# Kernel tuning notes

Hardware: AMD Instinct MI355X
Metric: run time of the kernel (lower is better)

Reference implementation:

```python
import jax, jax.numpy as jnp
import numpy as np
from jax import lax

NUM_TAGS = 19
IN_DIM = 202
HID = 100
B, T = 256, 512


def setup_inputs() -> dict:
    key = jax.random.key(0)
    ks = jax.random.split(key, 16)
    u = lambda k, shape, s: jax.random.uniform(k, shape, jnp.float32, -s, s)
    sh = 1.0 / np.sqrt(HID)
    sl = 1.0 / np.sqrt(2 * HID)
    x = jax.random.normal(ks[0], (B, T, IN_DIM), jnp.float32)
    lengths = jax.random.randint(ks[1], (B,), 1, T + 1)
    raw_tags = jax.random.randint(ks[2], (B, T), 0, NUM_TAGS)
    y = jnp.where(jnp.arange(T)[None, :] < lengths[:, None], raw_tags, -1)
    return dict(
        x=x, y=y,
        w_ih_f=u(ks[3], (HID, IN_DIM), sh), w_hh_f=u(ks[4], (HID, HID), sh),
        b_ih_f=u(ks[5], (HID,), sh), b_hh_f=u(ks[6], (HID,), sh),
        w_ih_b=u(ks[7], (HID, IN_DIM), sh), w_hh_b=u(ks[8], (HID, HID), sh),
        b_ih_b=u(ks[9], (HID,), sh), b_hh_b=u(ks[10], (HID,), sh),
        w_lin=u(ks[11], (NUM_TAGS, 2 * HID), sl), b_lin=u(ks[12], (NUM_TAGS,), sl),
        start_trans=u(ks[13], (NUM_TAGS,), 0.1),
        end_trans=u(ks[14], (NUM_TAGS,), 0.1),
        trans=u(ks[15], (NUM_TAGS, NUM_TAGS), 0.1),
    )


def _rnn_dir(x, w_ih, w_hh, b_ih, b_hh, reverse):
    # torch nn.RNN (tanh) scans over axis 0 of x (batch_first=False semantics)
    def step(h, xt):
        h = jnp.tanh(xt @ w_ih.T + b_ih + h @ w_hh.T + b_hh)
        return h, h
    h0 = jnp.zeros((x.shape[1], w_hh.shape[0]), x.dtype)
    _, hs = lax.scan(step, h0, x, reverse=reverse)
    return hs  # (S, N, HID)


def _emissions(x, w_ih_f, w_hh_f, b_ih_f, b_hh_f, w_ih_b, w_hh_b, b_ih_b, b_hh_b, w_lin, b_lin):
    hf = _rnn_dir(x, w_ih_f, w_hh_f, b_ih_f, b_hh_f, False)
    hb = _rnn_dir(x, w_ih_b, w_hh_b, b_ih_b, b_hh_b, True)
    h = jnp.concatenate([hf, hb], axis=-1)  # (B, T, 200)
    return jax.nn.softmax(h @ w_lin.T + b_lin, axis=2)  # (B, T, 19)


def _crf_llh(em, tags, mask, start, end, trans):
    # emissions (B,T,K) batch_first -> transpose to (T,B,*) for the scans
    em_t = jnp.swapaxes(em, 0, 1)
    tg = jnp.where(jnp.swapaxes(mask, 0, 1), jnp.swapaxes(tags, 0, 1), 0)
    mk = jnp.swapaxes(mask, 0, 1)
    mf = mk.astype(em.dtype)
    # numerator: gold path score
    s0 = start[tg[0]] + jnp.take_along_axis(em_t[0], tg[0][:, None], 1)[:, 0]
    def num_step(carry, inp):
        s, prev = carry
        e, t, m, mb = inp
        emit = jnp.take_along_axis(e, t[:, None], 1)[:, 0]
        s = s + (trans[prev, t] + emit) * m
        prev = jnp.where(mb, t, prev)  # track tag at last valid position
        return (s, prev), None
    (num, last), _ = lax.scan(num_step, (s0, tg[0]), (em_t[1:], tg[1:], mf[1:], mk[1:]))
    num = num + end[last]
    # denominator: masked forward algorithm
    def z_step(s, inp):
        e, mb = inp
        nxt = jax.nn.logsumexp(s[:, :, None] + trans[None] + e[:, None, :], axis=1)
        return jnp.where(mb[:, None], nxt, s), None
    z, _ = lax.scan(z_step, start + em_t[0], (em_t[1:], mk[1:]))
    logz = jax.nn.logsumexp(z + end, axis=1)
    return num - logz  # (B,) log-likelihood per sequence


def _viterbi(em, mask, start, end, trans):
    em_t = jnp.swapaxes(em, 0, 1)
    mk = jnp.swapaxes(mask, 0, 1)
    def fstep(s, inp):
        e, mb = inp
        cand = s[:, :, None] + trans[None] + e[:, None, :]  # (B,K,K)
        nxt = jnp.where(mb[:, None], jnp.max(cand, axis=1), s)
        return nxt, jnp.argmax(cand, axis=1)
    score, hist = lax.scan(fstep, start + em_t[0], (em_t[1:], mk[1:]))  # hist (T-1,B,K)
    best_last = jnp.argmax(score + end, axis=1)  # tag at each sequence end
    def bstep(tag, inp):
        h, mb = inp
        prev = jnp.take_along_axis(h, tag[:, None], 1)[:, 0]
        tag = jnp.where(mb, prev, tag)
        return tag, tag
    _, tags_bt = lax.scan(bstep, best_last, (hist, mk[1:]), reverse=True)  # (T-1,B), position order
    tags = jnp.concatenate([tags_bt, best_last[None]], axis=0)  # (T,B)
    tags = jnp.swapaxes(tags, 0, 1)
    return jnp.where(mask, tags, -1)  # pad with -1 like the torch pad_sequence


def reference(x, y, w_ih_f, w_hh_f, b_ih_f, b_hh_f, w_ih_b, w_hh_b, b_ih_b, b_hh_b, w_lin, b_lin, start_trans, end_trans, trans):
    mask = y != -1
    em = _emissions(x, w_ih_f, w_hh_f, b_ih_f, b_hh_f, w_ih_b, w_hh_b, b_ih_b, b_hh_b, w_lin, b_lin)
    loss = -jnp.sum(_crf_llh(em, y, mask, start_trans, end_trans, trans))  # reduction='sum'
    label = _viterbi(em, mask, start_trans, end_trans, trans)
    return loss, label
```

## Files before the change

kernel.cpp:

```cpp
#include <hip/hip_runtime.h>
#include <hip/hip_bf16.h>

#define B_ 256
#define T_ 512
#define IN_ 202
#define HID_ 100
#define K_ 19

typedef __attribute__((ext_vector_type(8))) short short8v;
typedef __attribute__((ext_vector_type(4))) float f32x4;

__device__ __forceinline__ float rl_f(float v, int l) {
  return __int_as_float(__builtin_amdgcn_readlane(__float_as_int(v), l));
}

__global__ __launch_bounds__(256, 1) void k_wprep(
    const float* __restrict__ wf, const float* __restrict__ wb,
    unsigned short* __restrict__ w3) {
  int idx = blockIdx.x * 256 + threadIdx.x;
  if (idx >= 224 * 224) return;
  int c = idx / 224, k = idx - (idx / 224) * 224;
  float v = 0.f;
  if (k < IN_) {
    if (c < 100) v = wf[c * IN_ + k];
    else if (c < 200) v = wb[(c - 100) * IN_ + k];
  }
  unsigned u0 = __float_as_uint(v) & 0xffff0000u;
  float r1 = v - __uint_as_float(u0);
  unsigned u1 = __float_as_uint(r1) & 0xffff0000u;
  float r2 = r1 - __uint_as_float(u1);
  w3[idx] = (unsigned short)(u0 >> 16);
  w3[50176 + idx] = (unsigned short)(u1 >> 16);
  w3[100352 + idx] = (unsigned short)(__float_as_uint(r2) >> 16);
}

__global__ __launch_bounds__(256, 2) void k_ih(
    const float* __restrict__ x, const unsigned short* __restrict__ w3,
    const float* __restrict__ bif, const float* __restrict__ bhf,
    const float* __restrict__ bib, const float* __restrict__ bhb,
    float* __restrict__ pre) {
  __shared__ float xs[256 * 36];
  __shared__ float bsum[224];
  int tid = threadIdx.x;
  int wv = tid >> 6, l = tid & 63;
  long row0 = (long)blockIdx.x * 256;
  for (int u = tid; u < 224; u += 256) {
    float bv = 0.f;
    if (u < 100) bv = bif[u] + bhf[u];
    else if (u < 200) bv = bib[u - 100] + bhb[u - 100];
    bsum[u] = bv;
  }
  int lr = l & 15;
  int kq = l >> 4;
  for (int g = 0; g < 2; g++) {
    f32x4 acc[4][7];
#pragma unroll
    for (int m = 0; m < 4; m++)
#pragma unroll
      for (int n = 0; n < 7; n++) acc[m][n] = (f32x4){0.f, 0.f, 0.f, 0.f};
    for (int ck = 0; ck < 7; ck++) {
      int k0 = ck * 32;
      __syncthreads();
#pragma unroll
      for (int i = 0; i < 16; i++) {
        int u = tid + i * 256;
        int r = u >> 4, kp = u & 15;
        int gk = k0 + 2 * kp;
        float2 v = make_float2(0.f, 0.f);
        if (gk < IN_) v = *(const float2*)(x + (row0 + r) * IN_ + gk);
        *(float2*)(&xs[r * 36 + 2 * kp]) = v;
      }
      __syncthreads();
      short8v A0[4], A1[4], A2[4];
#pragma unroll
      for (int m = 0; m < 4; m++) {
        const float* ap = &xs[(wv * 64 + m * 16 + lr) * 36 + kq * 8];
        float4 fa = *(const float4*)(ap);
        float4 fb = *(const float4*)(ap + 4);
        float f[8] = {fa.x, fa.y, fa.z, fa.w, fb.x, fb.y, fb.z, fb.w};
#pragma unroll
        for (int j = 0; j < 8; j++) {
          unsigned u0 = __float_as_uint(f[j]) & 0xffff0000u;
          float r1 = f[j] - __uint_as_float(u0);
          unsigned u1 = __float_as_uint(r1) & 0xffff0000u;
          float r2 = r1 - __uint_as_float(u1);
          A0[m][j] = (short)(u0 >> 16);
          A1[m][j] = (short)(u1 >> 16);
          A2[m][j] = (short)(__float_as_uint(r2) >> 16);
        }
      }
#pragma unroll
      for (int n = 0; n < 7; n++) {
        int col = (g * 7 + n) * 16 + lr;
        const unsigned short* bp = w3 + (long)col * 224 + k0 + kq * 8;
        short8v B0 = *(const short8v*)(bp);
        short8v B1 = *(const short8v*)(bp + 50176);
        short8v B2 = *(const short8v*)(bp + 100352);
#pragma unroll
        for (int m = 0; m < 4; m++) {
          f32x4 c = acc[m][n];
          c = __builtin_amdgcn_mfma_f32_16x16x32_bf16(A0[m], B0, c, 0, 0, 0);
          c = __builtin_amdgcn_mfma_f32_16x16x32_bf16(A0[m], B1, c, 0, 0, 0);
          c = __builtin_amdgcn_mfma_f32_16x16x32_bf16(A1[m], B0, c, 0, 0, 0);
          c = __builtin_amdgcn_mfma_f32_16x16x32_bf16(A0[m], B2, c, 0, 0, 0);
          c = __builtin_amdgcn_mfma_f32_16x16x32_bf16(A2[m], B0, c, 0, 0, 0);
          c = __builtin_amdgcn_mfma_f32_16x16x32_bf16(A1[m], B1, c, 0, 0, 0);
          c = __builtin_amdgcn_mfma_f32_16x16x32_bf16(A1[m], B2, c, 0, 0, 0);
          c = __builtin_amdgcn_mfma_f32_16x16x32_bf16(A2[m], B1, c, 0, 0, 0);
          acc[m][n] = c;
        }
      }
    }
#pragma unroll
    for (int m = 0; m < 4; m++) {
      long rbase = row0 + wv * 64 + m * 16 + kq * 4;
#pragma unroll
      for (int n = 0; n < 7; n++) {
        int col = (g * 7 + n) * 16 + lr;
        if (col < 200) {
          float bv = bsum[col];
#pragma unroll
          for (int r = 0; r < 4; r++)
            pre[(rbase + r) * 200 + col] = acc[m][n][r] + bv;
        }
      }
    }
  }
}

template <int KO, int KN, bool OW>
__device__ __forceinline__ void rnn_loop(
    float* __restrict__ p, long step, int row, bool owns,
    const float* __restrict__ w, float (*hb)[104], float* __restrict__ ps) {
  float wr[KN];
#pragma unroll
  for (int i = 0; i < KN / 4; i++) {
    float4 w4 = *(const float4*)(w + row * HID_ + KO + 4 * i);
    wr[4 * i + 0] = w4.x; wr[4 * i + 1] = w4.y;
    wr[4 * i + 2] = w4.z; wr[4 * i + 3] = w4.w;
  }
  float a = 0.f;
  if (OW) a = p[row];
  for (int s = 0; s < B_; s++) {
    int cur = s & 1;
    float a_next = 0.f;
    if (OW && s < B_ - 1) a_next = p[step + row];
    float ac0 = OW ? a : 0.f, ac1 = 0.f, ac2 = 0.f, ac3 = 0.f;
#pragma unroll
    for (int i = 0; i < KN / 4; i++) {
      float4 h4 = *(const float4*)(&hb[cur][KO + 4 * i]);
      ac0 = fmaf(h4.x, wr[4 * i + 0], ac0);
      ac1 = fmaf(h4.y, wr[4 * i + 1], ac1);
      ac2 = fmaf(h4.z, wr[4 * i + 2], ac2);
      ac3 = fmaf(h4.w, wr[4 * i + 3], ac3);
    }
    float partial = (ac0 + ac1) + (ac2 + ac3);
    if (!OW && owns) ps[row] = partial;
    __syncthreads();
    if (OW) {
      float hnew = tanhf(partial + ps[row]);
      if (owns) {
        hb[cur ^ 1][row] = hnew;
        p[row] = hnew;
      }
    }
    p += step;
    a = a_next;
    __syncthreads();
  }
}

__global__ __launch_bounds__(256, 4) void k_rnn(
    float* __restrict__ pre,
    const float* __restrict__ whf, const float* __restrict__ whb) {
  __shared__ float hb[2][104];
  __shared__ float ps[104];
  int bid = blockIdx.x;
  int dir = bid >> 9;
  int t = bid & 511;
  const float* w = dir ? whb : whf;
  int tid = threadIdx.x;
  int wv = tid >> 6, lane = tid & 63;
  int grp = wv >> 1;
  int khalf = wv & 1;
  int row = grp ? (64 + (lane < 36 ? lane : 35)) : lane;
  bool owns = grp ? (lane < 36) : true;
  long step = dir ? -(long)(T_ * 200) : (long)(T_ * 200);
  float* p = pre + ((long)(dir ? (B_ - 1) : 0) * T_ + t) * 200 + dir * 100;
  if (tid < 104) hb[0][tid] = 0.f;
  __syncthreads();
  if (khalf == 0) rnn_loop<0, 52, true >(p, step, row, owns, w, hb, ps);
  else            rnn_loop<52, 48, false>(p, step, row, owns, w, hb, ps);
}

__global__ __launch_bounds__(256, 4) void k_lin(
    const float* __restrict__ h, const float* __restrict__ wlin,
    const float* __restrict__ blin, float* __restrict__ em) {
  int tid = threadIdx.x;
  long r0 = ((long)blockIdx.x * 256 + tid) * 2;
  const float* h0 = h + r0 * 200;
  float acc0[K_], acc1[K_];
#pragma unroll
  for (int c = 0; c < K_; c++) { float bb = blin[c]; acc0[c] = bb; acc1[c] = bb; }
  for (int kk = 0; kk < 50; kk++) {
    float4 a = *(const float4*)(h0 + 4 * kk);
    float4 b = *(const float4*)(h0 + 200 + 4 * kk);
#pragma unroll
    for (int c = 0; c < K_; c++) {
      float4 wv = *(const float4*)(wlin + c * 200 + 4 * kk);
      acc0[c] += a.x * wv.x + a.y * wv.y + a.z * wv.z + a.w * wv.w;
      acc1[c] += b.x * wv.x + b.y * wv.y + b.z * wv.z + b.w * wv.w;
    }
  }
  float mx0 = acc0[0], mx1 = acc1[0];
#pragma unroll
  for (int c = 1; c < K_; c++) { mx0 = fmaxf(mx0, acc0[c]); mx1 = fmaxf(mx1, acc1[c]); }
  float s0 = 0.f, s1 = 0.f;
#pragma unroll
  for (int c = 0; c < K_; c++) {
    acc0[c] = __expf(acc0[c] - mx0); s0 += acc0[c];
    acc1[c] = __expf(acc1[c] - mx1); s1 += acc1[c];
  }
  float i0 = 1.f / s0, i1 = 1.f / s1;
  float* e0 = em + r0 * K_;
#pragma unroll
  for (int c = 0; c < K_; c++) { e0[c] = acc0[c] * i0; e0[K_ + c] = acc1[c] * i1; }
}

__global__ __launch_bounds__(128, 1) void k_crf(
    const float* __restrict__ em, const int* __restrict__ y,
    const float* __restrict__ st_g, const float* __restrict__ en_g,
    const float* __restrict__ tr_g,
    float* __restrict__ part, int* __restrict__ cnt,
    float* __restrict__ out) {
  __shared__ __align__(16) float es[T_ * K_];
  __shared__ int ys[T_];
  __shared__ float trs[K_ * K_];
  __shared__ float st[K_], en[K_];
  __shared__ unsigned char hl[511 * K_ + 13];
  __shared__ __align__(16) float zbuf[2][20];
  __shared__ __align__(16) float vbuf[2][20];
  int b = blockIdx.x;
  int tid = threadIdx.x;
  int wv = tid >> 6, lane = tid & 63;
  const float4* eb4 = (const float4*)(em + (long)b * T_ * K_);
  for (int u = tid; u < T_ * K_ / 4; u += 128) ((float4*)es)[u] = eb4[u];
  for (int u = tid; u < T_; u += 128) ys[u] = y[b * T_ + u];
  for (int u = tid; u < K_ * K_; u += 128) trs[u] = tr_g[u];
  if (tid < K_) { st[tid] = st_g[tid]; en[tid] = en_g[tid]; }
  if (tid == 19) { zbuf[0][19] = -1e30f; zbuf[1][19] = -1e30f; vbuf[0][19] = -1e30f; vbuf[1][19] = -1e30f; }
  __syncthreads();
  int lmin = T_;
  for (int u = lane; u < T_; u += 64)
    if (ys[u] == -1 && u < lmin) lmin = u;
#pragma unroll
  for (int off = 32; off; off >>= 1) {
    int o = __shfl_xor(lmin, off, 64);
    lmin = lmin < o ? lmin : o;
  }
  int len = lmin;

  int jj = lane < K_ ? lane : K_ - 1;
  bool act = lane < K_;
  float enr[20];
#pragma unroll
  for (int q = 0; q < 5; q++) {
    float4 e4 = (q < 4) ? *(const float4*)(&en[4 * q])
                        : make_float4(en[16], en[17], en[18], -1e30f);
    enr[4 * q] = e4.x; enr[4 * q + 1] = e4.y; enr[4 * q + 2] = e4.z; enr[4 * q + 3] = e4.w;
  }

  if (wv == 0) {
    float gacc = 0.f;
    for (int t = 1 + lane; t < len; t += 64)
      gacc += trs[ys[t - 1] * K_ + ys[t]] + es[t * K_ + ys[t]];
#pragma unroll
    for (int off = 32; off; off >>= 1) gacc += __shfl_xor(gacc, off, 64);
    int y0 = ys[0], ylast = ys[len - 1];
    float num = st[y0] + es[y0] + gacc + en[ylast];
    float E[K_];
#pragma unroll
    for (int i = 0; i < K_; i++) E[i] = __expf(trs[i * K_ + jj]);
    if (act) zbuf[0][lane] = st[jj] + es[jj];
    asm volatile("s_waitcnt lgkmcnt(0)" ::: "memory");
    for (int t = 1; t < len; t++) {
      int cur = (t - 1) & 1;
      float zr[20];
#pragma unroll
      for (int q = 0; q < 5; q++) {
        float4 z4 = *(const float4*)(&zbuf[cur][4 * q]);
        zr[4 * q] = z4.x; zr[4 * q + 1] = z4.y; zr[4 * q + 2] = z4.z; zr[4 * q + 3] = z4.w;
      }
      float e = es[t * K_ + jj];
      float s = zr[0];
      float p0 = 1.f;
      float a0 = p0 * E[0], a1 = 0.f, a2 = 0.f, a3 = 0.f;
#pragma unroll
      for (int i = 1; i < K_; i++) {
        float pz = __expf(zr[i] - s);
        if ((i & 3) == 1)      a1 = fmaf(pz, E[i], a1);
        else if ((i & 3) == 2) a2 = fmaf(pz, E[i], a2);
        else if ((i & 3) == 3) a3 = fmaf(pz, E[i], a3);
        else                   a0 = fmaf(pz, E[i], a0);
      }
      float nz = e + s + __logf((a0 + a1) + (a2 + a3));
      if (act) zbuf[cur ^ 1][lane] = nz;
      asm volatile("s_waitcnt lgkmcnt(0)" ::: "memory");
    }
    {
      int cur = (len - 1) & 1;
      float zr[20];
#pragma unroll
      for (int q = 0; q < 5; q++) {
        float4 z4 = *(const float4*)(&zbuf[cur][4 * q]);
        zr[4 * q] = z4.x; zr[4 * q + 1] = z4.y; zr[4 * q + 2] = z4.z; zr[4 * q + 3] = z4.w;
      }
      float zf[K_];
#pragma unroll
      for (int i = 0; i < K_; i++) zf[i] = zr[i] + enr[i];
      float m2 = zf[0];
#pragma unroll
      for (int i = 1; i < K_; i++) m2 = fmaxf(m2, zf[i]);
      float sm = 0.f;
#pragma unroll
      for (int i = 0; i < K_; i++) sm += __expf(zf[i] - m2);
      if (lane == 0) part[b] = m2 + __logf(sm) - num;
    }
    int old = -1;
    if (lane == 0) { __threadfence(); old = atomicAdd(cnt, 1); }
    old = __shfl(old, 0, 64);
    if (old == B_ - 1) {
      __threadfence();
      float s = 0.f;
      for (int u = lane; u < B_; u += 64) s += part[u];
#pragma unroll
      for (int off = 32; off; off >>= 1) s += __shfl_xor(s, off, 64);
      if (lane == 0) out[0] = s;
    }
  } else {
    float Tt[K_];
#pragma unroll
    for (int i = 0; i < K_; i++) Tt[i] = trs[i * K_ + jj];
    if (act) vbuf[0][lane] = st[jj] + es[jj];
    asm volatile("s_waitcnt lgkmcnt(0)" ::: "memory");
    for (int t = 1; t < len; t++) {
      int cur = (t - 1) & 1;
      float vr[20];
#pragma unroll
      for (int q = 0; q < 5; q++) {
        float4 v4 = *(const float4*)(&vbuf[cur][4 * q]);
        vr[4 * q] = v4.x; vr[4 * q + 1] = v4.y; vr[4 * q + 2] = v4.z; vr[4 * q + 3] = v4.w;
      }
      float e = es[t * K_ + jj];
      float b0 = -1e30f, b1 = -1e30f, b2 = -1e30f, b3 = -1e30f;
      int a0 = 0, a1 = 5, a2 = 10, a3 = 15;
#pragma unroll
      for (int i = 0; i < 5; i++)  { float c = vr[i] + Tt[i]; if (c > b0) { b0 = c; a0 = i; } }
#pragma unroll
      for (int i = 5; i < 10; i++) { float c = vr[i] + Tt[i]; if (c > b1) { b1 = c; a1 = i; } }
#pragma unroll
      for (int i = 10; i < 15; i++){ float c = vr[i] + Tt[i]; if (c > b2) { b2 = c; a2 = i; } }
#pragma unroll
      for (int i = 15; i < 19; i++){ float c = vr[i] + Tt[i]; if (c > b3) { b3 = c; a3 = i; } }
      if (b1 > b0) { b0 = b1; a0 = a1; }
      if (b2 > b0) { b0 = b2; a0 = a2; }
      if (b3 > b0) { b0 = b3; a0 = a3; }
      if (act) {
        hl[(t - 1) * K_ + lane] = (unsigned char)a0;
        vbuf[cur ^ 1][lane] = b0 + e;
      }
      asm volatile("s_waitcnt lgkmcnt(0)" ::: "memory");
    }
    int aa;
    {
      int cur = (len - 1) & 1;
      float vr[20];
#pragma unroll
      for (int q = 0; q < 5; q++) {
        float4 v4 = *(const float4*)(&vbuf[cur][4 * q]);
        vr[4 * q] = v4.x; vr[4 * q + 1] = v4.y; vr[4 * q + 2] = v4.z; vr[4 * q + 3] = v4.w;
      }
      float bb = vr[0] + enr[0]; aa = 0;
#pragma unroll
      for (int i = 1; i < K_; i++) {
        float c = vr[i] + enr[i];
        if (c > bb) { bb = c; aa = i; }
      }
    }
    float* ob = out + 1 + (long)b * T_;
    for (int u = lane; u < T_; u += 64)
      if (u >= len) ob[u] = -1.f;
    int tag = aa;
    if (lane == 0) ob[len - 1] = (float)tag;
    int vc = (act && len >= 2) ? (int)hl[(len - 2) * K_ + lane] : 0;
    for (int ti = len - 2; ti >= 0; ti--) {
      int vn = 0;
      if (ti > 0 && act) vn = (int)hl[(ti - 1) * K_ + lane];
      int ts = __builtin_amdgcn_readfirstlane(tag);
      tag = __builtin_amdgcn_readlane(vc, ts);
      if (lane == 0) ob[ti] = (float)tag;
      vc = vn;
    }
  }
}

extern "C" void kernel_launch(void* const* d_in, const int* in_sizes, int n_in,
                              void* d_out, int out_size, void* d_ws, size_t ws_size,
                              hipStream_t stream) {
  const float* x      = (const float*)d_in[0];
  const int*   y      = (const int*)d_in[1];
  const float* w_ih_f = (const float*)d_in[2];
  const float* w_hh_f = (const float*)d_in[3];
  const float* b_ih_f = (const float*)d_in[4];
  const float* b_hh_f = (const float*)d_in[5];
  const float* w_ih_b = (const float*)d_in[6];
  const float* w_hh_b = (const float*)d_in[7];
  const float* b_ih_b = (const float*)d_in[8];
  const float* b_hh_b = (const float*)d_in[9];
  const float* w_lin  = (const float*)d_in[10];
  const float* b_lin  = (const float*)d_in[11];
  const float* st     = (const float*)d_in[12];
  const float* en     = (const float*)d_in[13];
  const float* trans  = (const float*)d_in[14];

  char* ws = (char*)d_ws;
  const size_t PRE_OFF  = 0;
  const size_t EM_OFF   = 104857600;
  const size_t PART_OFF = EM_OFF + 9961472;
  const size_t CNT_OFF  = PART_OFF + 1024;
  float* PRE  = (float*)(ws + PRE_OFF);
  float* EM   = (float*)(ws + EM_OFF);
  float* PART = (float*)(ws + PART_OFF);
  int*   CNT  = (int*)(ws + CNT_OFF);
  unsigned short* W3 = (unsigned short*)(ws + EM_OFF);
  float* out  = (float*)d_out;

  hipMemsetAsync((void*)CNT, 0, sizeof(int), stream);
  k_wprep<<<196, 256, 0, stream>>>(w_ih_f, w_ih_b, W3);
  k_ih<<<512, 256, 0, stream>>>(x, W3, b_ih_f, b_hh_f, b_ih_b, b_hh_b, PRE);
  k_rnn<<<1024, 256, 0, stream>>>(PRE, w_hh_f, w_hh_b);
  k_lin<<<256, 256, 0, stream>>>(PRE, w_lin, b_lin, EM);
  k_crf<<<256, 128, 0, stream>>>(EM, y, st, en, trans, PART, CNT, out);
}
```

Before: 652.3 us.

## Batch recurrent RNN steps onto MFMA with split-bf16 hidden weights

Rewrites the recurrent RNN kernel so that each block handles 16 independent sequences at once and computes the hidden-state update as a 16x112x128 matrix product. It uses bf16 MFMA with a two-term bf16 split of both the hidden state and W_hh to keep near-fp32 accuracy. A new prep kernel splits and pads W_hh, and the grid shrinks from 1024 scalar-FMA blocks to 64 MFMA blocks. The aim is to remove the per-sequence scalar dot products and the double barrier per step. In exchange, only 64 blocks run the 256-step serial chain, so parallelism is much lower and each step depends on the MFMA latency chain.

```diff
diff --git a/kernel.cpp b/kernel.cpp
--- a/kernel.cpp
+++ b/kernel.cpp
@@ -32,6 +32,24 @@
   w3[idx] = (unsigned short)(u0 >> 16);
   w3[50176 + idx] = (unsigned short)(u1 >> 16);
   w3[100352 + idx] = (unsigned short)(__float_as_uint(r2) >> 16);
+}
+
+__global__ __launch_bounds__(256, 1) void k_whprep(
+    const float* __restrict__ whf, const float* __restrict__ whb,
+    unsigned short* __restrict__ wh) {
+  int idx = blockIdx.x * 256 + threadIdx.x;
+  if (idx >= 4 * 112 * 128) return;
+  int k = idx & 127;
+  int rest = idx >> 7;
+  int c = rest % 112;
+  int dp = rest / 112;
+  int dir = dp >> 1, p = dp & 1;
+  float v = 0.f;
+  if (c < 100 && k < 100) v = (dir ? whb : whf)[c * 100 + k];
+  unsigned u0 = __float_as_uint(v) & 0xffff0000u;
+  float r1 = v - __uint_as_float(u0);
+  unsigned u1 = __float_as_uint(r1) & 0xffff0000u;
+  wh[idx] = p ? (unsigned short)(u1 >> 16) : (unsigned short)(u0 >> 16);
 }
 
 __global__ __launch_bounds__(256, 2) void k_ih(
@@ -128,69 +146,107 @@
   }
 }
 
-template <int KO, int KN, bool OW>
-__device__ __forceinline__ void rnn_loop(
-    float* __restrict__ p, long step, int row, bool owns,
-    const float* __restrict__ w, float (*hb)[104], float* __restrict__ ps) {
-  float wr[KN];
-#pragma unroll
-  for (int i = 0; i < KN / 4; i++) {
-    float4 w4 = *(const float4*)(w + row * HID_ + KO + 4 * i);
-    wr[4 * i + 0] = w4.x; wr[4 * i + 1] = w4.y;
-    wr[4 * i + 2] = w4.z; wr[4 * i + 3] = w4.w;
-  }
-  float a = 0.f;
-  if (OW) a = p[row];
+__global__ __launch_bounds__(256) void k_rnn(
+    float* __restrict__ pre, const unsigned short* __restrict__ wh) {
+  __shared__ unsigned short Hp[2][2][16][136];
+  int bid = blockIdx.x;
+  int dir = bid >> 5;
+  int t0 = (bid & 31) * 16;
+  int tid = threadIdx.x;
+  int wv = tid >> 6, l = tid & 63;
+  int lr = l & 15, g = l >> 4;
+  int ntiles = (wv < 3) ? 2 : 1;
+  int nbase = (wv < 3) ? 2 * wv : 6;
+  short8v B0[2][4], B1[2][4];
+#pragma unroll
+  for (int n = 0; n < 2; n++) {
+    if (n < ntiles) {
+      int col = (nbase + n) * 16 + lr;
+      const unsigned short* b0p = wh + ((long)(dir * 2 + 0) * 112 + col) * 128 + g * 8;
+      const unsigned short* b1p = wh + ((long)(dir * 2 + 1) * 112 + col) * 128 + g * 8;
+#pragma unroll
+      for (int q = 0; q < 4; q++) {
+        B0[n][q] = *(const short8v*)(b0p + q * 32);
+        B1[n][q] = *(const short8v*)(b1p + q * 32);
+      }
+    }
+  }
+  for (int u = tid; u < 2 * 2 * 16 * 136; u += 256) ((unsigned short*)Hp)[u] = 0;
+  long stepoff = dir ? -(long)T_ * 200 : (long)T_ * 200;
+  float* base = pre + ((long)(dir ? (B_ - 1) : 0) * T_ + t0) * 200 + dir * 100;
+  int goff[2][4];
+  bool gok[2][4];
+#pragma unroll
+  for (int n = 0; n < 2; n++)
+#pragma unroll
+    for (int r = 0; r < 4; r++) {
+      int col = (nbase + n) * 16 + lr;
+      int row = g * 4 + r;
+      goff[n][r] = row * 200 + col;
+      gok[n][r] = (n < ntiles) && (col < 100);
+    }
+  float pc[2][4];
+#pragma unroll
+  for (int n = 0; n < 2; n++)
+#pragma unroll
+    for (int r = 0; r < 4; r++)
+      pc[n][r] = gok[n][r] ? base[goff[n][r]] : 0.f;
+  __syncthreads();
+  int cur = 0;
+  float* bp = base;
   for (int s = 0; s < B_; s++) {
-    int cur = s & 1;
-    float a_next = 0.f;
-    if (OW && s < B_ - 1) a_next = p[step + row];
-    float ac0 = OW ? a : 0.f, ac1 = 0.f, ac2 = 0.f, ac3 = 0.f;
-#pragma unroll
-    for (int i = 0; i < KN / 4; i++) {
-      float4 h4 = *(const float4*)(&hb[cur][KO + 4 * i]);
-      ac0 = fmaf(h4.x, wr[4 * i + 0], ac0);
-      ac1 = fmaf(h4.y, wr[4 * i + 1], ac1);
-      ac2 = fmaf(h4.z, wr[4 * i + 2], ac2);
-      ac3 = fmaf(h4.w, wr[4 * i + 3], ac3);
-    }
-    float partial = (ac0 + ac1) + (ac2 + ac3);
-    if (!OW && owns) ps[row] = partial;
+    float pn[2][4];
+#pragma unroll
+    for (int n = 0; n < 2; n++)
+#pragma unroll
+      for (int r = 0; r < 4; r++)
+        pn[n][r] = (s < B_ - 1 && gok[n][r]) ? bp[stepoff + goff[n][r]] : 0.f;
+    short8v A0[4], A1[4];
+#pragma unroll
+    for (int q = 0; q < 4; q++) {
+      A0[q] = *(const short8v*)&Hp[cur][0][lr][q * 32 + g * 8];
+      A1[q] = *(const short8v*)&Hp[cur][1][lr][q * 32 + g * 8];
+    }
+#pragma unroll
+    for (int n = 0; n < 2; n++) {
+      if (n < ntiles) {
+        f32x4 aca = {pc[n][0], pc[n][1], pc[n][2], pc[n][3]};
+        f32x4 acb = {0.f, 0.f, 0.f, 0.f};
+#pragma unroll
+        for (int q = 0; q < 2; q++) {
+          aca = __builtin_amdgcn_mfma_f32_16x16x32_bf16(A0[q], B0[n][q], aca, 0, 0, 0);
+          aca = __builtin_amdgcn_mfma_f32_16x16x32_bf16(A0[q], B1[n][q], aca, 0, 0, 0);
+          aca = __builtin_amdgcn_mfma_f32_16x16x32_bf16(A1[q], B0[n][q], aca, 0, 0, 0);
+          aca = __builtin_amdgcn_mfma_f32_16x16x32_bf16(A1[q], B1[n][q], aca, 0, 0, 0);
+        }
+#pragma unroll
+        for (int q = 2; q < 4; q++) {
+          acb = __builtin_amdgcn_mfma_f32_16x16x32_bf16(A0[q], B0[n][q], acb, 0, 0, 0);
+          acb = __builtin_amdgcn_mfma_f32_16x16x32_bf16(A0[q], B1[n][q], acb, 0, 0, 0);
+          acb = __builtin_amdgcn_mfma_f32_16x16x32_bf16(A1[q], B0[n][q], acb, 0, 0, 0);
+          acb = __builtin_amdgcn_mfma_f32_16x16x32_bf16(A1[q], B1[n][q], acb, 0, 0, 0);
+        }
+#pragma unroll
+        for (int r = 0; r < 4; r++) {
+          float hv = tanhf(aca[r] + acb[r]);
+          if (gok[n][r]) bp[goff[n][r]] = hv;
+          unsigned u0 = __float_as_uint(hv) & 0xffff0000u;
+          float r1 = hv - __uint_as_float(u0);
+          unsigned u1 = __float_as_uint(r1) & 0xffff0000u;
+          int row = g * 4 + r, col = (nbase + n) * 16 + lr;
+          Hp[cur ^ 1][0][row][col] = (unsigned short)(u0 >> 16);
+          Hp[cur ^ 1][1][row][col] = (unsigned short)(u1 >> 16);
+        }
+      }
+    }
     __syncthreads();
-    if (OW) {
-      float hnew = tanhf(partial + ps[row]);
-      if (owns) {
-        hb[cur ^ 1][row] = hnew;
-        p[row] = hnew;
-      }
-    }
-    p += step;
-    a = a_next;
-    __syncthreads();
-  }
-}
-
-__global__ __launch_bounds__(256, 4) void k_rnn(
-    float* __restrict__ pre,
-    const float* __restrict__ whf, const float* __restrict__ whb) {
-  __shared__ float hb[2][104];
-  __shared__ float ps[104];
-  int bid = blockIdx.x;
-  int dir = bid >> 9;
-  int t = bid & 511;
-  const float* w = dir ? whb : whf;
-  int tid = threadIdx.x;
-  int wv = tid >> 6, lane = tid & 63;
-  int grp = wv >> 1;
-  int khalf = wv & 1;
-  int row = grp ? (64 + (lane < 36 ? lane : 35)) : lane;
-  bool owns = grp ? (lane < 36) : true;
-  long step = dir ? -(long)(T_ * 200) : (long)(T_ * 200);
-  float* p = pre + ((long)(dir ? (B_ - 1) : 0) * T_ + t) * 200 + dir * 100;
-  if (tid < 104) hb[0][tid] = 0.f;
-  __syncthreads();
-  if (khalf == 0) rnn_loop<0, 52, true >(p, step, row, owns, w, hb, ps);
-  else            rnn_loop<52, 48, false>(p, step, row, owns, w, hb, ps);
+    cur ^= 1;
+    bp += stepoff;
+#pragma unroll
+    for (int n = 0; n < 2; n++)
+#pragma unroll
+      for (int r = 0; r < 4; r++) pc[n][r] = pn[n][r];
+  }
 }
 
 __global__ __launch_bounds__(256, 4) void k_lin(
@@ -293,8 +349,7 @@
       }
       float e = es[t * K_ + jj];
       float s = zr[0];
-      float p0 = 1.f;
-      float a0 = p0 * E[0], a1 = 0.f, a2 = 0.f, a3 = 0.f;
+      float a0 = E[0], a1 = 0.f, a2 = 0.f, a3 = 0.f;
 #pragma unroll
       for (int i = 1; i < K_; i++) {
         float pz = __expf(zr[i] - s);
@@ -428,17 +483,20 @@
   const size_t EM_OFF   = 104857600;
   const size_t PART_OFF = EM_OFF + 9961472;
   const size_t CNT_OFF  = PART_OFF + 1024;
+  const size_t WH_OFF   = PART_OFF + 4096;
   float* PRE  = (float*)(ws + PRE_OFF);
   float* EM   = (float*)(ws + EM_OFF);
   float* PART = (float*)(ws + PART_OFF);
   int*   CNT  = (int*)(ws + CNT_OFF);
   unsigned short* W3 = (unsigned short*)(ws + EM_OFF);
+  unsigned short* WH = (unsigned short*)(ws + WH_OFF);
   float* out  = (float*)d_out;
 
   hipMemsetAsync((void*)CNT, 0, sizeof(int), stream);
   k_wprep<<<196, 256, 0, stream>>>(w_ih_f, w_ih_b, W3);
+  k_whprep<<<224, 256, 0, stream>>>(w_hh_f, w_hh_b, WH);
   k_ih<<<512, 256, 0, stream>>>(x, W3, b_ih_f, b_hh_f, b_ih_b, b_hh_b, PRE);
-  k_rnn<<<1024, 256, 0, stream>>>(PRE, w_hh_f, w_hh_b);
+  k_rnn<<<64, 256, 0, stream>>>(PRE, WH);
   k_lin<<<256, 256, 0, stream>>>(PRE, w_lin, b_lin, EM);
   k_crf<<<256, 128, 0, stream>>>(EM, y, st, en, trans, PART, CNT, out);
 }
```

Result: slower. 936.1 us (+43.5%).

## Run CRF forward recursion in linear space with exponent-based rescaling

Applied to the files above, without the earlier changes.

The CRF partition-function recursion now keeps probabilities in linear space instead of log space. Each step is a plain dot product with exp(trans), times exp(emission), renormalised by a power of two taken from the first element's exponent bits. The per-step 18 exps and one log become a single exp for the next emission, which is prefetched. In exchange, precision relies on the first state not underflowing relative to the others, and the accumulated exponent count is folded back in only at the end.

```diff
diff --git a/kernel.cpp b/kernel.cpp
--- a/kernel.cpp
+++ b/kernel.cpp
@@ -248,7 +248,7 @@
   for (int u = tid; u < T_; u += 128) ys[u] = y[b * T_ + u];
   for (int u = tid; u < K_ * K_; u += 128) trs[u] = tr_g[u];
   if (tid < K_) { st[tid] = st_g[tid]; en[tid] = en_g[tid]; }
-  if (tid == 19) { zbuf[0][19] = -1e30f; zbuf[1][19] = -1e30f; vbuf[0][19] = -1e30f; vbuf[1][19] = -1e30f; }
+  if (tid == 19) { zbuf[0][19] = 0.f; zbuf[1][19] = 0.f; vbuf[0][19] = -1e30f; vbuf[1][19] = -1e30f; }
   __syncthreads();
   int lmin = T_;
   for (int u = lane; u < T_; u += 64)
@@ -278,53 +278,52 @@
     for (int off = 32; off; off >>= 1) gacc += __shfl_xor(gacc, off, 64);
     int y0 = ys[0], ylast = ys[len - 1];
     float num = st[y0] + es[y0] + gacc + en[ylast];
-    float E[K_];
-#pragma unroll
-    for (int i = 0; i < K_; i++) E[i] = __expf(trs[i * K_ + jj]);
-    if (act) zbuf[0][lane] = st[jj] + es[jj];
+    float Ecol[K_];
+#pragma unroll
+    for (int i = 0; i < K_; i++) Ecol[i] = __expf(trs[i * K_ + jj]);
+    if (act) zbuf[0][lane] = __expf(st[jj] + es[jj]);
     asm volatile("s_waitcnt lgkmcnt(0)" ::: "memory");
+    int kacc = 0;
+    float ee = __expf(es[K_ + jj]);
     for (int t = 1; t < len; t++) {
       int cur = (t - 1) & 1;
-      float zr[20];
+      float pr[20];
 #pragma unroll
       for (int q = 0; q < 5; q++) {
         float4 z4 = *(const float4*)(&zbuf[cur][4 * q]);
-        zr[4 * q] = z4.x; zr[4 * q + 1] = z4.y; zr[4 * q + 2] = z4.z; zr[4 * q + 3] = z4.w;
-      }
-      float e = es[t * K_ + jj];
-      float s = zr[0];
-      float p0 = 1.f;
-      float a0 = p0 * E[0], a1 = 0.f, a2 = 0.f, a3 = 0.f;
-#pragma unroll
-      for (int i = 1; i < K_; i++) {
-        float pz = __expf(zr[i] - s);
-        if ((i & 3) == 1)      a1 = fmaf(pz, E[i], a1);
-        else if ((i & 3) == 2) a2 = fmaf(pz, E[i], a2);
-        else if ((i & 3) == 3) a3 = fmaf(pz, E[i], a3);
-        else                   a0 = fmaf(pz, E[i], a0);
-      }
-      float nz = e + s + __logf((a0 + a1) + (a2 + a3));
+        pr[4 * q] = z4.x; pr[4 * q + 1] = z4.y; pr[4 * q + 2] = z4.z; pr[4 * q + 3] = z4.w;
+      }
+      int tn = (t + 1 < T_) ? t + 1 : T_ - 1;
+      float e_next = es[tn * K_ + jj];
+      unsigned pb = __float_as_uint(pr[0]);
+      int ex = (int)((pb >> 23) & 0xff);
+      float scale = __uint_as_float((unsigned)(254 - ex) << 23);
+      kacc += ex - 127;
+      float a0 = 0.f, a1 = 0.f, a2 = 0.f, a3 = 0.f;
+#pragma unroll
+      for (int i = 0; i < K_; i++) {
+        if ((i & 3) == 0)      a0 = fmaf(pr[i], Ecol[i], a0);
+        else if ((i & 3) == 1) a1 = fmaf(pr[i], Ecol[i], a1);
+        else if ((i & 3) == 2) a2 = fmaf(pr[i], Ecol[i], a2);
+        else                   a3 = fmaf(pr[i], Ecol[i], a3);
+      }
+      float nz = (((a0 + a1) + (a2 + a3)) * ee) * scale;
       if (act) zbuf[cur ^ 1][lane] = nz;
       asm volatile("s_waitcnt lgkmcnt(0)" ::: "memory");
+      ee = __expf(e_next);
     }
     {
       int cur = (len - 1) & 1;
-      float zr[20];
+      float pr[20];
 #pragma unroll
       for (int q = 0; q < 5; q++) {
         float4 z4 = *(const float4*)(&zbuf[cur][4 * q]);
-        zr[4 * q] = z4.x; zr[4 * q + 1] = z4.y; zr[4 * q + 2] = z4.z; zr[4 * q + 3] = z4.w;
-      }
-      float zf[K_];
-#pragma unroll
-      for (int i = 0; i < K_; i++) zf[i] = zr[i] + enr[i];
-      float m2 = zf[0];
-#pragma unroll
-      for (int i = 1; i < K_; i++) m2 = fmaxf(m2, zf[i]);
+        pr[4 * q] = z4.x; pr[4 * q + 1] = z4.y; pr[4 * q + 2] = z4.z; pr[4 * q + 3] = z4.w;
+      }
       float sm = 0.f;
 #pragma unroll
-      for (int i = 0; i < K_; i++) sm += __expf(zf[i] - m2);
-      if (lane == 0) part[b] = m2 + __logf(sm) - num;
+      for (int i = 0; i < K_; i++) sm += pr[i] * __expf(enr[i]);
+      if (lane == 0) part[b] = __logf(sm) + (float)kacc * 0.6931471805599453f - num;
     }
     int old = -1;
     if (lane == 0) { __threadfence(); old = atomicAdd(cnt, 1); }
```

Measured after the change: 659.2 us. About the same (+1.1%).
